# Kernel tuning notes

Hardware: AMD Instinct MI355X
Metric: run time of the kernel (lower is better)

The kernel has to match this reference:

```python
import jax, jax.numpy as jnp
import numpy as np


def setup_inputs() -> dict:
    key = jax.random.key(0)
    k1, k2 = jax.random.split(key)
    imgs = jax.random.normal(k1, (16, 64, 64, 64), dtype=jnp.float32)
    # matches np.random.normal(0, 0.01, (1, inCs, outCs, filtSize, filtSize, 2))
    filts = 0.01 * jax.random.normal(k2, (1, 64, 64, 3, 3, 2), dtype=jnp.float32)
    return {"imgs": imgs, "filts": filts}


def reference(imgs, filts):
    # imgs:  [B, inC, H, W] real
    # filts: [1, inC, outC, fs, fs, 2] (real/imag planes)
    B, inC, H, W = imgs.shape
    fs = filts.shape[3]
    # zero-pad image to S = H + fs - 1 (full linear-conv FFT size)
    imgs_p = jnp.pad(imgs, ((0, 0), (0, 0), (0, fs - 1), (0, fs - 1)))
    img_f = jnp.fft.fftn(imgs_p, axes=(-2, -1))  # [B, inC, S, S] complex64
    # complex filter, padded to same FFT size
    fc = (filts[0, ..., 0] + 1j * filts[0, ..., 1]).astype(jnp.complex64)  # [inC, outC, fs, fs]
    fc_p = jnp.pad(fc, ((0, 0), (0, 0), (0, H - 1), (0, W - 1)))
    filt_f = jnp.fft.fftn(fc_p, axes=(-2, -1))  # [inC, outC, S, S]
    # Karatsuba complex multiply + sum over inC == complex contraction over inC.
    # Fused as one einsum instead of materializing [B,inC,outC,S,S] intermediates.
    out_f = jnp.einsum('bihw,iohw->bohw', img_f, filt_f)  # [B, outC, S, S]
    out = jnp.fft.ifftn(out_f, axes=(-2, -1))
    # crop [1:-1, 1:-1] and take real part, as in the torch module
    return out[:, :, 1:-1, 1:-1].real.astype(imgs.dtype)
```

## Files before the change

### kernel.cpp

```cpp
#include <hip/hip_runtime.h>


typedef _Float16 f16x8 __attribute__((ext_vector_type(8)));
typedef float    f32x4 __attribute__((ext_vector_type(4)));

#define NB 16
#define NC 64
#define NH 64
#define NW 64
#define CHUNKS 528
#define SLAB_BYTES (CHUNKS * 16)
#define WF_HALFS (9 * 2 * 4 * 64 * 8)

__global__ __launch_bounds__(256) void prep_w(const float* __restrict__ filts,
                                              _Float16* __restrict__ wf) {
    const int f = blockIdx.x * 256 + threadIdx.x;
    if (f >= WF_HALFS) return;
    const int e  = f & 7;
    const int l  = (f >> 3) & 63;
    const int n  = (f >> 9) & 3;
    const int kc = (f >> 11) & 1;
    const int t  = f >> 12;
    const int i  = kc * 32 + (l >> 4) * 8 + e;
    const int o  = n * 16 + (l & 15);
    const int ky = t / 3, kx = t % 3;
    wf[f] = (_Float16)filts[(((i * 64 + o) * 3 + ky) * 3 + kx) * 2];
}

__global__ __launch_bounds__(128, 2) void conv_row(const float* __restrict__ imgs,
                                                   const _Float16* __restrict__ wf,
                                                   float* __restrict__ out) {
    __shared__ uint4 ldsb[3 * SLAB_BYTES / 16];
    char* lds = reinterpret_cast<char*>(ldsb);
    const int bid = blockIdx.x;
    const int swz = ((bid & 7) << 7) | (bid >> 3);
    const int b   = swz >> 6;
    const int y   = swz & 63;
    const int tid = threadIdx.x;
    const int w   = tid >> 6;
    const int l   = tid & 63;
    const int h   = l >> 4;
    const int r   = l & 15;

    if (tid < 48) {
        const int sl  = tid >> 4;
        const int rem = tid & 15;
        const int ci  = rem >> 1;
        const int xp2 = (rem & 1) ? 65 : 0;
        const int c2  = xp2 * 8 + (ci ^ (xp2 & 7));
        f16x8 z;
        #pragma unroll
        for (int k = 0; k < 8; ++k) z[k] = (_Float16)0.f;
        *reinterpret_cast<f16x8*>(lds + sl * SLAB_BYTES + c2 * 16) = z;
    }

    for (int g = w; g < 24; g += 2) {
        const int sl = g >> 3;
        const int ci = g & 7;
        const int yy = y - 1 + sl;
        f16x8 v;
        if ((unsigned)yy < (unsigned)NH) {
            const float* src = imgs + (((size_t)(b * NC + ci * 8)) * NH + yy) * NW + l;
            #pragma unroll
            for (int k = 0; k < 8; ++k) v[k] = (_Float16)src[(size_t)k * NH * NW];
        } else {
            #pragma unroll
            for (int k = 0; k < 8; ++k) v[k] = (_Float16)0.f;
        }
        const int xp = l + 1;
        const int chunk = xp * 8 + (ci ^ (xp & 7));
        *reinterpret_cast<f16x8*>(lds + sl * SLAB_BYTES + chunk * 16) = v;
    }
    __syncthreads();

    f32x4 acc[4][2];
    #pragma unroll
    for (int m = 0; m < 4; ++m)
        #pragma unroll
        for (int n = 0; n < 2; ++n)
            acc[m][n] = f32x4{0.f, 0.f, 0.f, 0.f};

    #pragma unroll
    for (int ky = 0; ky < 3; ++ky) {
        const char* slab = lds + (2 - ky) * SLAB_BYTES;
        #pragma unroll
        for (int kx = 0; kx < 3; ++kx) {
            const _Float16* wft = wf + (size_t)(ky * 3 + kx) * (2 * 4 * 64 * 8);
            #pragma unroll
            for (int kc = 0; kc < 2; ++kc) {
                f16x8 a[4], bb[2];
                #pragma unroll
                for (int m = 0; m < 4; ++m) {
                    const int xp = m * 16 + r + 2 - kx;
                    const int chunk = xp * 8 + (((kc << 2) + h) ^ (xp & 7));
                    a[m] = *reinterpret_cast<const f16x8*>(slab + chunk * 16);
                }
                #pragma unroll
                for (int n = 0; n < 2; ++n)
                    bb[n] = *reinterpret_cast<const f16x8*>(
                        wft + ((size_t)((kc << 2) + (w * 2 + n)) * 64 + l) * 8);
                #pragma unroll
                for (int m = 0; m < 4; ++m)
                    #pragma unroll
                    for (int n = 0; n < 2; ++n)
                        acc[m][n] = __builtin_amdgcn_mfma_f32_16x16x32_f16(a[m], bb[n], acc[m][n], 0, 0, 0);
            }
        }
    }

    #pragma unroll
    for (int m = 0; m < 4; ++m) {
        const int x0 = m * 16 + h * 4;
        #pragma unroll
        for (int n = 0; n < 2; ++n) {
            const int o = w * 32 + n * 16 + r;
            *reinterpret_cast<f32x4*>(out + (((size_t)(b * 64 + o) * 64 + y) * 64) + x0) = acc[m][n];
        }
    }
}

extern "C" void kernel_launch(void* const* d_in, const int* in_sizes, int n_in,
                              void* d_out, int out_size, void* d_ws, size_t ws_size,
                              hipStream_t stream) {
    const float* imgs  = (const float*)d_in[0];
    const float* filts = (const float*)d_in[1];
    float* out = (float*)d_out;
    _Float16* wfb = (_Float16*)d_ws;

    hipLaunchKernelGGL(prep_w, dim3((WF_HALFS + 255) / 256), dim3(256), 0, stream, filts, wfb);
    hipLaunchKernelGGL(conv_row, dim3(NB * NH), dim3(128), 0, stream, imgs, wfb, out);
}
```

Baseline: 22.50 us.

## Process four output rows per block to cut redundant input-row loads

Each block now covers four consecutive output rows using six shared input slabs instead of three slabs per single row, which reduces redundant global reads and fp16 conversions of the image halo rows. The eight waves split work by row and x-half, and each wave computes all 64 output channels. The grid shrinks to 256 blocks of 512 threads, trading occupancy and latency hiding for reuse. Global loads are batched before conversion to raise memory-level parallelism.

```diff
diff --git a/kernel.cpp b/kernel.cpp
--- a/kernel.cpp
+++ b/kernel.cpp
@@ -27,22 +27,21 @@
     wf[f] = (_Float16)filts[(((i * 64 + o) * 3 + ky) * 3 + kx) * 2];
 }
 
-__global__ __launch_bounds__(128, 2) void conv_row(const float* __restrict__ imgs,
-                                                   const _Float16* __restrict__ wf,
-                                                   float* __restrict__ out) {
-    __shared__ uint4 ldsb[3 * SLAB_BYTES / 16];
-    char* lds = reinterpret_cast<char*>(ldsb);
+__global__ __launch_bounds__(512, 1) void conv_direct(const float* __restrict__ imgs,
+                                                      const _Float16* __restrict__ wf,
+                                                      float* __restrict__ out) {
+    __shared__ char lds[6 * SLAB_BYTES];
     const int bid = blockIdx.x;
-    const int swz = ((bid & 7) << 7) | (bid >> 3);
-    const int b   = swz >> 6;
-    const int y   = swz & 63;
+    const int swz = ((bid & 7) << 5) | (bid >> 3);
+    const int b   = swz >> 4;
+    const int y0  = (swz & 15) << 2;
     const int tid = threadIdx.x;
     const int w   = tid >> 6;
     const int l   = tid & 63;
     const int h   = l >> 4;
     const int r   = l & 15;
 
-    if (tid < 48) {
+    if (tid < 96) {
         const int sl  = tid >> 4;
         const int rem = tid & 15;
         const int ci  = rem >> 1;
@@ -54,66 +53,75 @@
         *reinterpret_cast<f16x8*>(lds + sl * SLAB_BYTES + c2 * 16) = z;
     }
 
-    for (int g = w; g < 24; g += 2) {
-        const int sl = g >> 3;
-        const int ci = g & 7;
-        const int yy = y - 1 + sl;
-        f16x8 v;
+    #pragma unroll
+    for (int j = 0; j < 6; ++j) {
+        const int job = w + j * 8;
+        const int sl  = job >> 3;
+        const int ci  = job & 7;
+        const int yy  = y0 - 1 + sl;
+        float fr[8];
         if ((unsigned)yy < (unsigned)NH) {
             const float* src = imgs + (((size_t)(b * NC + ci * 8)) * NH + yy) * NW + l;
             #pragma unroll
-            for (int k = 0; k < 8; ++k) v[k] = (_Float16)src[(size_t)k * NH * NW];
+            for (int k = 0; k < 8; ++k) fr[k] = src[(size_t)k * NH * NW];
         } else {
             #pragma unroll
-            for (int k = 0; k < 8; ++k) v[k] = (_Float16)0.f;
+            for (int k = 0; k < 8; ++k) fr[k] = 0.f;
         }
+        f16x8 v;
+        #pragma unroll
+        for (int k = 0; k < 8; ++k) v[k] = (_Float16)fr[k];
         const int xp = l + 1;
         const int chunk = xp * 8 + (ci ^ (xp & 7));
         *reinterpret_cast<f16x8*>(lds + sl * SLAB_BYTES + chunk * 16) = v;
     }
     __syncthreads();
 
-    f32x4 acc[4][2];
+    const int row = w >> 1;
+    const int xh  = w & 1;
+
+    f32x4 acc[2][4];
     #pragma unroll
-    for (int m = 0; m < 4; ++m)
+    for (int m = 0; m < 2; ++m)
         #pragma unroll
-        for (int n = 0; n < 2; ++n)
+        for (int n = 0; n < 4; ++n)
             acc[m][n] = f32x4{0.f, 0.f, 0.f, 0.f};
 
     #pragma unroll
     for (int ky = 0; ky < 3; ++ky) {
-        const char* slab = lds + (2 - ky) * SLAB_BYTES;
+        const char* slab = lds + (row + 2 - ky) * SLAB_BYTES;
         #pragma unroll
         for (int kx = 0; kx < 3; ++kx) {
             const _Float16* wft = wf + (size_t)(ky * 3 + kx) * (2 * 4 * 64 * 8);
             #pragma unroll
             for (int kc = 0; kc < 2; ++kc) {
-                f16x8 a[4], bb[2];
+                f16x8 a[2], bb[4];
                 #pragma unroll
-                for (int m = 0; m < 4; ++m) {
-                    const int xp = m * 16 + r + 2 - kx;
+                for (int m = 0; m < 2; ++m) {
+                    const int xp = xh * 32 + m * 16 + r + 2 - kx;
                     const int chunk = xp * 8 + (((kc << 2) + h) ^ (xp & 7));
                     a[m] = *reinterpret_cast<const f16x8*>(slab + chunk * 16);
                 }
                 #pragma unroll
-                for (int n = 0; n < 2; ++n)
+                for (int n = 0; n < 4; ++n)
                     bb[n] = *reinterpret_cast<const f16x8*>(
-                        wft + ((size_t)((kc << 2) + (w * 2 + n)) * 64 + l) * 8);
+                        wft + ((size_t)((kc << 2) + n) * 64 + l) * 8);
                 #pragma unroll
-                for (int m = 0; m < 4; ++m)
+                for (int m = 0; m < 2; ++m)
                     #pragma unroll
-                    for (int n = 0; n < 2; ++n)
+                    for (int n = 0; n < 4; ++n)
                         acc[m][n] = __builtin_amdgcn_mfma_f32_16x16x32_f16(a[m], bb[n], acc[m][n], 0, 0, 0);
             }
         }
     }
 
+    const int y = y0 + row;
     #pragma unroll
-    for (int m = 0; m < 4; ++m) {
-        const int x0 = m * 16 + h * 4;
+    for (int m = 0; m < 2; ++m) {
+        const int x0 = xh * 32 + m * 16 + h * 4;
         #pragma unroll
-        for (int n = 0; n < 2; ++n) {
-            const int o = w * 32 + n * 16 + r;
+        for (int n = 0; n < 4; ++n) {
+            const int o = n * 16 + r;
             *reinterpret_cast<f32x4*>(out + (((size_t)(b * 64 + o) * 64 + y) * 64) + x0) = acc[m][n];
         }
     }
@@ -128,5 +136,5 @@
     _Float16* wfb = (_Float16*)d_ws;
 
     hipLaunchKernelGGL(prep_w, dim3((WF_HALFS + 255) / 256), dim3(256), 0, stream, filts, wfb);
-    hipLaunchKernelGGL(conv_row, dim3(NB * NH), dim3(128), 0, stream, imgs, wfb, out);
+    hipLaunchKernelGGL(conv_direct, dim3(256), dim3(512), 0, stream, imgs, wfb, out);
 }
```

Result: faster. 20.91 us (-7.0%).
